# Performance work log

Measured on AMD Instinct MI355X. Metric: run time of the kernel, lower is better.

The kernel has to match this reference:

```python
import jax, jax.numpy as jnp
import numpy as np

BS = 128          # block size hard-coded in linear_deepseek_v3
FP8_MAX = 448.0   # float8_e4m3fn max-normal, used by act_quant_deepseek_v3


def act_quant(x):
    """Per-token, per-128-column-block activation quantization.
    x: [T, K] -> (xq [T, K], scale [T, K//BS]) with xq = x / scale per block."""
    T, K = x.shape
    xb = x.reshape(T, K // BS, BS)
    amax = jnp.max(jnp.abs(xb), axis=-1)              # [T, K//BS]
    scale = amax / FP8_MAX + 1e-12
    xq = (xb / scale[:, :, None]).reshape(T, K)
    return xq, scale


def linear_dsv3(x, wq, w_scale):
    """y = dequant(act_quant(x)) @ dequant(wq, w_scale).T
    x: [T, K]; wq: [N, K] fp8-style values; w_scale: [N//BS, K//BS]."""
    T, K = x.shape
    N = wq.shape[0]
    xq, xs = act_quant(x)
    # dequantized activations [T, K]
    xdq = (xq.reshape(T, K // BS, BS) * xs[:, :, None]).reshape(T, K)
    # dequantized weights [N, K] via 128x128 block scales
    wdq = (wq.reshape(N // BS, BS, K // BS, BS) * w_scale[:, None, :, None]).reshape(N, K)
    return xdq @ wdq.T


def setup_inputs() -> dict:
    key = jax.random.key(0)
    ks = jax.random.split(key, 4)
    DIM, INTER = 4096, 14336

    def make_qweight(k, n, m):
        w = jax.random.normal(k, (n, m), dtype=jnp.float32) * 0.02
        wb = w.reshape(n // BS, BS, m // BS, BS)
        amax = jnp.max(jnp.abs(wb), axis=(1, 3))       # [n//BS, m//BS]
        scale = amax / FP8_MAX + 1e-12
        wq = (wb / scale[:, None, :, None]).reshape(n, m)
        return wq, scale

    x = jax.random.normal(ks[0], (2, 1024, DIM), dtype=jnp.float32)
    w1, w1_scale = make_qweight(ks[1], INTER, DIM)
    w3, w3_scale = make_qweight(ks[2], INTER, DIM)
    w2, w2_scale = make_qweight(ks[3], DIM, INTER)
    return {"x": x, "w1": w1, "w1_scale": w1_scale, "w3": w3,
            "w3_scale": w3_scale, "w2": w2, "w2_scale": w2_scale}


def reference(x, w1, w1_scale, w3, w3_scale, w2, w2_scale):
    B, S, D = x.shape
    xf = x.reshape(-1, D)                               # [T, D]
    g = linear_dsv3(xf, w1, w1_scale)                   # gate  [T, INTER]
    u = linear_dsv3(xf, w3, w3_scale)                   # up    [T, INTER]
    h = jax.nn.silu(g) * u                              # SwiGLU
    y = linear_dsv3(h, w2, w2_scale)                    # down  [T, D]
    return y.reshape(B, S, D)
```

## Files before the change

kernel.cpp:

```cpp
#include <hip/hip_runtime.h>
#include <hip/hip_bf16.h>
#include <stdint.h>

typedef __attribute__((ext_vector_type(8))) short short8;
typedef __attribute__((ext_vector_type(4))) float f32x4;
typedef __attribute__((ext_vector_type(8))) unsigned short u16x8;

static __device__ __forceinline__ unsigned short f2bf(float f) {
  union { float f; unsigned int u; } c; c.f = f;
  unsigned int u = c.u;
  u += 0x7FFFu + ((u >> 16) & 1u);
  return (unsigned short)(u >> 16);
}
static __device__ __forceinline__ float bf2f(unsigned short h) {
  union { unsigned int u; float f; } c; c.u = ((unsigned int)h) << 16;
  return c.f;
}
static __device__ __forceinline__ f32x4 mfma_bf16(short8 a, short8 b, f32x4 c) {
  return __builtin_amdgcn_mfma_f32_16x16x32_bf16(a, b, c, 0, 0, 0);
}
static __device__ __forceinline__ void gl_lds16(const void* g, void* lds) {
  __builtin_amdgcn_global_load_lds(
      (const __attribute__((address_space(1))) void*)(unsigned long long)(uintptr_t)g,
      (__attribute__((address_space(3))) void*)(unsigned int)(uintptr_t)lds,
      16, 0, 0);
}

__global__ void k_cvt_w(const float* __restrict__ w, const float* __restrict__ s,
                        unsigned short* __restrict__ o, int N, int K) {
  const int KB = K >> 7;
  const size_t total = ((size_t)N * K) >> 3;
  for (size_t i = (size_t)blockIdx.x * blockDim.x + threadIdx.x; i < total;
       i += (size_t)gridDim.x * blockDim.x) {
    const size_t e = i << 3;
    const int n = (int)(e / K);
    const int k = (int)(e % K);
    const float sc = s[(n >> 7) * KB + (k >> 7)];
    f32x4 a = *(const f32x4*)(w + e);
    f32x4 b = *(const f32x4*)(w + e + 4);
    u16x8 q;
    #pragma unroll
    for (int j = 0; j < 4; ++j) { q[j] = f2bf(a[j] * sc); q[4 + j] = f2bf(b[j] * sc); }
    *(u16x8*)(o + e) = q;
  }
}

__global__ void k_cvt_x(const float* __restrict__ x, unsigned short* __restrict__ o,
                        size_t total8) {
  for (size_t i = (size_t)blockIdx.x * blockDim.x + threadIdx.x; i < total8;
       i += (size_t)gridDim.x * blockDim.x) {
    const size_t e = i << 3;
    f32x4 a = *(const f32x4*)(x + e);
    f32x4 b = *(const f32x4*)(x + e + 4);
    u16x8 q;
    #pragma unroll
    for (int j = 0; j < 4; ++j) { q[j] = f2bf(a[j]); q[4 + j] = f2bf(b[j]); }
    *(u16x8*)(o + e) = q;
  }
}

template<int NB, int EPI>
__global__ __launch_bounds__(512, 2)
void k_gemm256(const unsigned short* __restrict__ A,
               const unsigned short* __restrict__ B,
               const unsigned short* Gin,
               void* Out,
               int M, int N, int K) {
  constexpr int BN   = NB * 128;
  constexpr int NREP = NB * 2;
  __shared__ unsigned short lds[65536];

  const int tid  = threadIdx.x;
  const int lane = tid & 63;
  const int wid  = tid >> 6;
  const int wm   = wid >> 2;
  const int wn   = wid & 3;
  const int lr   = lane & 15;
  const int kg   = lane >> 4;
  const int xr   = (lr & 7) << 4;

  const int nwg = gridDim.x;
  const int per = nwg >> 3;
  const int wg  = (int)blockIdx.x;
  const int swz = (wg & 7) * per + (wg >> 3);
  const int bm  = swz & 7;
  const int bn  = swz >> 3;

  const int r0   = tid >> 3;
  const int colb = ((tid & 7) ^ ((tid >> 3) & 7)) << 4;
  const size_t ldb = (size_t)K * 2;

  const char* gA = (const char*)A + (size_t)bm * 256 * ldb;
  const char* gB = (const char*)B + (size_t)bn * BN * ldb;

  const int NT = K >> 6;

  auto stage = [&](int t) {
    const size_t kb = (size_t)t * 128;
    #pragma unroll
    for (int h = 0; h < 2; ++h) {
      unsigned short* d = lds + (((2 * t + h) & 3) * 8192) + wid * 512;
      const char* s = gA + (size_t)(h * 128 + r0) * ldb + kb + colb;
      gl_lds16(s,            d);
      gl_lds16(s + 64 * ldb, d + 4096);
    }
    #pragma unroll
    for (int h = 0; h < NB; ++h) {
      unsigned short* d = lds + 32768 + (((NB * t + h) & 3) * 8192) + wid * 512;
      const char* s = gB + (size_t)(h * 128 + r0) * ldb + kb + colb;
      gl_lds16(s,            d);
      gl_lds16(s + 64 * ldb, d + 4096);
    }
  };

  f32x4 acc[8][NREP];
  #pragma unroll
  for (int m = 0; m < 8; ++m)
    #pragma unroll
    for (int n = 0; n < NREP; ++n)
      #pragma unroll
      for (int e = 0; e < 4; ++e) acc[m][n][e] = 0.0f;

  const int wrow0 = (NB == 2) ? (wn & 1) * 64 : wn * 32;
  const int bhalf = (NB == 2) ? (wn >> 1) : 0;

  stage(0);
  stage(1);

  for (int t = 0; t < NT; ++t) {
    if (t == NT - 1) {
      asm volatile("s_waitcnt vmcnt(0)" ::: "memory");
    } else if constexpr (NB == 2) {
      asm volatile("s_waitcnt vmcnt(8)" ::: "memory");
    } else {
      asm volatile("s_waitcnt vmcnt(6)" ::: "memory");
    }
    __builtin_amdgcn_s_barrier();
    __builtin_amdgcn_sched_barrier(0);

    const char* ab = (const char*)lds + (((2 * t + wm) & 3) * 16384);
    const char* bb = (const char*)lds + 65536 + (((NB * t + bhalf) & 3) * 16384);

    short8 a0[8], b0[NREP], a1[8], b1[NREP];
    #pragma unroll
    for (int m = 0; m < 8; ++m)
      a0[m] = *(const short8*)(ab + ((((m * 16 + lr) * 128) + kg * 16) ^ xr));
    #pragma unroll
    for (int n = 0; n < NREP; ++n)
      b0[n] = *(const short8*)(bb + ((((wrow0 + n * 16 + lr) * 128) + kg * 16) ^ xr));
    #pragma unroll
    for (int m = 0; m < 8; ++m)
      #pragma unroll
      for (int n = 0; n < NREP; ++n)
        acc[m][n] = mfma_bf16(a0[m], b0[n], acc[m][n]);

    #pragma unroll
    for (int m = 0; m < 8; ++m)
      a1[m] = *(const short8*)(ab + ((((m * 16 + lr) * 128) + 64 + kg * 16) ^ xr));
    #pragma unroll
    for (int n = 0; n < NREP; ++n)
      b1[n] = *(const short8*)(bb + ((((wrow0 + n * 16 + lr) * 128) + 64 + kg * 16) ^ xr));

    asm volatile("s_waitcnt lgkmcnt(0)" ::: "memory");
    __builtin_amdgcn_s_barrier();
    __builtin_amdgcn_sched_barrier(0);
    if (t + 2 < NT) stage(t + 2);
    __builtin_amdgcn_sched_barrier(0);

    #pragma unroll
    for (int m = 0; m < 8; ++m)
      #pragma unroll
      for (int n = 0; n < NREP; ++n)
        acc[m][n] = mfma_bf16(a1[m], b1[n], acc[m][n]);
  }

  const int growb = bm * 256 + wm * 128 + kg * 4;
  const int gcolb = bn * BN + wn * (BN / 4) + lr;
  #pragma unroll
  for (int m = 0; m < 8; ++m)
    #pragma unroll
    for (int n = 0; n < NREP; ++n)
      #pragma unroll
      for (int j = 0; j < 4; ++j) {
        const size_t idx = (size_t)(growb + m * 16 + j) * N + (gcolb + n * 16);
        if constexpr (EPI == 0) {
          ((unsigned short*)Out)[idx] = f2bf(acc[m][n][j]);
        } else if constexpr (EPI == 1) {
          const float gv = bf2f(Gin[idx]);
          const float sg = gv / (1.0f + __expf(-gv));
          ((unsigned short*)Out)[idx] = f2bf(sg * acc[m][n][j]);
        } else {
          ((float*)Out)[idx] = acc[m][n][j];
        }
      }
}

extern "C" void kernel_launch(void* const* d_in, const int* in_sizes, int n_in,
                              void* d_out, int out_size, void* d_ws, size_t ws_size,
                              hipStream_t stream) {
  const float* x   = (const float*)d_in[0];
  const float* w1  = (const float*)d_in[1];
  const float* w1s = (const float*)d_in[2];
  const float* w3  = (const float*)d_in[3];
  const float* w3s = (const float*)d_in[4];
  const float* w2  = (const float*)d_in[5];
  const float* w2s = (const float*)d_in[6];
  float* y = (float*)d_out;

  const int D = 4096, I = 14336;
  const int T = in_sizes[0] / D;

  const size_t xbB = (size_t)T * D * 2;
  const size_t wB  = (size_t)I * D * 2;
  const size_t gB_ = (size_t)T * I * 2;

  char* ws = (char*)d_ws;
  unsigned short* xb  = (unsigned short*)(ws);
  unsigned short* w1b = (unsigned short*)(ws + xbB);
  unsigned short* w3b = (unsigned short*)(ws + xbB + wB);
  unsigned short* w2b = (unsigned short*)(ws + xbB + 2 * wB);
  unsigned short* g   = (unsigned short*)(ws + xbB + 3 * wB);

  k_cvt_x<<<2048, 256, 0, stream>>>(x, xb, ((size_t)T * D) >> 3);
  k_cvt_w<<<2048, 256, 0, stream>>>(w1, w1s, w1b, I, D);
  k_cvt_w<<<2048, 256, 0, stream>>>(w3, w3s, w3b, I, D);
  k_cvt_w<<<2048, 256, 0, stream>>>(w2, w2s, w2b, D, I);

  k_gemm256<2, 0><<<dim3((T / 256) * (I / 256)), dim3(512), 0, stream>>>(
      xb, w1b, nullptr, g, T, I, D);
  k_gemm256<2, 1><<<dim3((T / 256) * (I / 256)), dim3(512), 0, stream>>>(
      xb, w3b, g, g, T, I, D);
  k_gemm256<1, 2><<<dim3((T / 256) * (D / 128)), dim3(512), 0, stream>>>(
      g, w2b, nullptr, y, T, D, I);
}
```

Before: 907.2 us.

## Restructure GEMM main loop into 8-phase ping-pong schedule with interleaved staging

```diff
diff --git a/kernel.cpp b/kernel.cpp
--- a/kernel.cpp
+++ b/kernel.cpp
@@ -59,16 +59,57 @@
   }
 }
 
+#define PH_MID() do { \
+    __builtin_amdgcn_sched_barrier(0); \
+    __builtin_amdgcn_s_barrier(); \
+    asm volatile("s_waitcnt lgkmcnt(0)" ::: "memory"); \
+    __builtin_amdgcn_sched_barrier(0); \
+    __builtin_amdgcn_s_setprio(1); \
+  } while (0)
+#define PH_END() do { \
+    __builtin_amdgcn_s_setprio(0); \
+    __builtin_amdgcn_sched_barrier(0); \
+    __builtin_amdgcn_s_barrier(); \
+  } while (0)
+
+#define READ_A(d, mh) do { \
+    const char* _ba = (const char*)lds + ((d) * 2 + wm) * 16384; \
+    _Pragma("unroll") \
+    for (int f = 0; f < 4; ++f) { \
+      aF[0][f] = *(const short8*)(_ba + ((((mh) * 64 + f * 16 + lr) * 128 + kg * 16) ^ xr)); \
+      aF[1][f] = *(const short8*)(_ba + ((((mh) * 64 + f * 16 + lr) * 128 + 64 + kg * 16) ^ xr)); \
+    } } while (0)
+#define READ_B(d, nh, bF) do { \
+    const char* _bb = (const char*)lds + ABYTES + ((d) * NBH + bhalf) * 16384; \
+    _Pragma("unroll") \
+    for (int f = 0; f < NH2; ++f) { \
+      bF[0][f] = *(const short8*)(_bb + (((wrow0 + ((nh) * NH2 + f) * 16 + lr) * 128 + kg * 16) ^ xr)); \
+      bF[1][f] = *(const short8*)(_bb + (((wrow0 + ((nh) * NH2 + f) * 16 + lr) * 128 + 64 + kg * 16) ^ xr)); \
+    } } while (0)
+#define MFMA_Q(mh, nh, bF) do { \
+    _Pragma("unroll") \
+    for (int m = 0; m < 4; ++m) \
+      _Pragma("unroll") \
+      for (int n = 0; n < NH2; ++n) { \
+        acc[(mh) * 4 + m][(nh) * NH2 + n] = \
+            mfma_bf16(aF[0][m], bF[0][n], acc[(mh) * 4 + m][(nh) * NH2 + n]); \
+        acc[(mh) * 4 + m][(nh) * NH2 + n] = \
+            mfma_bf16(aF[1][m], bF[1][n], acc[(mh) * 4 + m][(nh) * NH2 + n]); \
+      } } while (0)
+
 template<int NB, int EPI>
 __global__ __launch_bounds__(512, 2)
-void k_gemm256(const unsigned short* __restrict__ A,
-               const unsigned short* __restrict__ B,
-               const unsigned short* Gin,
-               void* Out,
-               int M, int N, int K) {
-  constexpr int BN   = NB * 128;
-  constexpr int NREP = NB * 2;
-  __shared__ unsigned short lds[65536];
+void k_gemm8p(const unsigned short* __restrict__ A,
+              const unsigned short* __restrict__ B,
+              const unsigned short* Gin,
+              void* Out,
+              int M, int N, int K) {
+  constexpr int BN     = NB * 128;
+  constexpr int NREP   = NB * 2;
+  constexpr int NH2    = NREP / 2;
+  constexpr int NBH    = NB;
+  constexpr int ABYTES = 65536;
+  __shared__ unsigned short lds[(NB == 2) ? 65536 : 49152];
 
   const int tid  = threadIdx.x;
   const int lane = tid & 63;
@@ -93,24 +134,20 @@
   const char* gA = (const char*)A + (size_t)bm * 256 * ldb;
   const char* gB = (const char*)B + (size_t)bn * BN * ldb;
 
-  const int NT = K >> 6;
-
-  auto stage = [&](int t) {
-    const size_t kb = (size_t)t * 128;
-    #pragma unroll
-    for (int h = 0; h < 2; ++h) {
-      unsigned short* d = lds + (((2 * t + h) & 3) * 8192) + wid * 512;
-      const char* s = gA + (size_t)(h * 128 + r0) * ldb + kb + colb;
-      gl_lds16(s,            d);
-      gl_lds16(s + 64 * ldb, d + 4096);
-    }
-    #pragma unroll
-    for (int h = 0; h < NB; ++h) {
-      unsigned short* d = lds + 32768 + (((NB * t + h) & 3) * 8192) + wid * 512;
-      const char* s = gB + (size_t)(h * 128 + r0) * ldb + kb + colb;
-      gl_lds16(s,            d);
-      gl_lds16(s + 64 * ldb, d + 4096);
-    }
+  const int wrow0 = (NB == 2) ? (wn & 1) * 64 : wn * 32;
+  const int bhalf = (NB == 2) ? (wn >> 1) : 0;
+
+  auto stageA = [&](int t, int h) {
+    unsigned short* d = lds + ((t & 1) * 2 + h) * 8192 + wid * 512;
+    const char* s = gA + (size_t)(h * 128 + r0) * ldb + (size_t)t * 128 + colb;
+    gl_lds16(s, d);
+    gl_lds16(s + 64 * ldb, d + 4096);
+  };
+  auto stageB = [&](int t, int h) {
+    unsigned short* d = lds + (ABYTES / 2) + ((t & 1) * NBH + h) * 8192 + wid * 512;
+    const char* s = gB + (size_t)(h * 128 + r0) * ldb + (size_t)t * 128 + colb;
+    gl_lds16(s, d);
+    gl_lds16(s + 64 * ldb, d + 4096);
   };
 
   f32x4 acc[8][NREP];
@@ -121,57 +158,70 @@
       #pragma unroll
       for (int e = 0; e < 4; ++e) acc[m][n][e] = 0.0f;
 
-  const int wrow0 = (NB == 2) ? (wn & 1) * 64 : wn * 32;
-  const int bhalf = (NB == 2) ? (wn >> 1) : 0;
-
-  stage(0);
-  stage(1);
-
-  for (int t = 0; t < NT; ++t) {
-    if (t == NT - 1) {
+  short8 aF[2][4], bF0[2][NH2], bF1[2][NH2];
+
+  const int NP = K >> 7;
+
+  stageB(0, 0); if constexpr (NB == 2) stageB(0, 1);
+  stageA(0, 0); stageA(0, 1);
+  stageB(1, 0); if constexpr (NB == 2) stageB(1, 1);
+  stageA(1, 0); stageA(1, 1);
+  if constexpr (NB == 2) asm volatile("s_waitcnt vmcnt(8)" ::: "memory");
+  else                   asm volatile("s_waitcnt vmcnt(6)" ::: "memory");
+  __builtin_amdgcn_sched_barrier(0);
+  __builtin_amdgcn_s_barrier();
+
+  for (int i = 0; i < NP; ++i) {
+    const int t0 = 2 * i, t1 = 2 * i + 1;
+    const bool more = (i + 1 < NP);
+
+    READ_A(0, 0);
+    READ_B(0, 0, bF0);
+    if (i > 0) stageA(t1, 1);
+    PH_MID(); MFMA_Q(0, 0, bF0); PH_END();
+
+    READ_B(0, 1, bF1);
+    PH_MID(); MFMA_Q(0, 1, bF1); PH_END();
+
+    READ_A(0, 1);
+    if (more) stageB(t0 + 2, 0);
+    PH_MID(); MFMA_Q(1, 1, bF1); PH_END();
+
+    if (more) { if constexpr (NB == 2) stageB(t0 + 2, 1); stageA(t0 + 2, 0); }
+    PH_MID(); MFMA_Q(1, 0, bF0);
+    __builtin_amdgcn_s_setprio(0);
+    __builtin_amdgcn_sched_barrier(0);
+    if (more) {
+      if constexpr (NB == 2) asm volatile("s_waitcnt vmcnt(6)" ::: "memory");
+      else                   asm volatile("s_waitcnt vmcnt(4)" ::: "memory");
+    } else {
       asm volatile("s_waitcnt vmcnt(0)" ::: "memory");
-    } else if constexpr (NB == 2) {
-      asm volatile("s_waitcnt vmcnt(8)" ::: "memory");
-    } else {
-      asm volatile("s_waitcnt vmcnt(6)" ::: "memory");
     }
+    __builtin_amdgcn_sched_barrier(0);
     __builtin_amdgcn_s_barrier();
-    __builtin_amdgcn_sched_barrier(0);
-
-    const char* ab = (const char*)lds + (((2 * t + wm) & 3) * 16384);
-    const char* bb = (const char*)lds + 65536 + (((NB * t + bhalf) & 3) * 16384);
-
-    short8 a0[8], b0[NREP], a1[8], b1[NREP];
-    #pragma unroll
-    for (int m = 0; m < 8; ++m)
-      a0[m] = *(const short8*)(ab + ((((m * 16 + lr) * 128) + kg * 16) ^ xr));
-    #pragma unroll
-    for (int n = 0; n < NREP; ++n)
-      b0[n] = *(const short8*)(bb + ((((wrow0 + n * 16 + lr) * 128) + kg * 16) ^ xr));
-    #pragma unroll
-    for (int m = 0; m < 8; ++m)
-      #pragma unroll
-      for (int n = 0; n < NREP; ++n)
-        acc[m][n] = mfma_bf16(a0[m], b0[n], acc[m][n]);
-
-    #pragma unroll
-    for (int m = 0; m < 8; ++m)
-      a1[m] = *(const short8*)(ab + ((((m * 16 + lr) * 128) + 64 + kg * 16) ^ xr));
-    #pragma unroll
-    for (int n = 0; n < NREP; ++n)
-      b1[n] = *(const short8*)(bb + ((((wrow0 + n * 16 + lr) * 128) + 64 + kg * 16) ^ xr));
-
-    asm volatile("s_waitcnt lgkmcnt(0)" ::: "memory");
+
+    READ_A(1, 0);
+    READ_B(1, 0, bF0);
+    if (more) stageA(t0 + 2, 1);
+    PH_MID(); MFMA_Q(0, 0, bF0); PH_END();
+
+    READ_B(1, 1, bF1);
+    PH_MID(); MFMA_Q(0, 1, bF1); PH_END();
+
+    READ_A(1, 1);
+    if (more) stageB(t1 + 2, 0);
+    PH_MID(); MFMA_Q(1, 1, bF1); PH_END();
+
+    if (more) { if constexpr (NB == 2) stageB(t1 + 2, 1); stageA(t1 + 2, 0); }
+    PH_MID(); MFMA_Q(1, 0, bF0);
+    __builtin_amdgcn_s_setprio(0);
+    __builtin_amdgcn_sched_barrier(0);
+    if (more) {
+      if constexpr (NB == 2) asm volatile("s_waitcnt vmcnt(6)" ::: "memory");
+      else                   asm volatile("s_waitcnt vmcnt(4)" ::: "memory");
+    }
+    __builtin_amdgcn_sched_barrier(0);
     __builtin_amdgcn_s_barrier();
-    __builtin_amdgcn_sched_barrier(0);
-    if (t + 2 < NT) stage(t + 2);
-    __builtin_amdgcn_sched_barrier(0);
-
-    #pragma unroll
-    for (int m = 0; m < 8; ++m)
-      #pragma unroll
-      for (int n = 0; n < NREP; ++n)
-        acc[m][n] = mfma_bf16(a1[m], b1[n], acc[m][n]);
   }
 
   const int growb = bm * 256 + wm * 128 + kg * 4;
@@ -212,7 +262,6 @@
 
   const size_t xbB = (size_t)T * D * 2;
   const size_t wB  = (size_t)I * D * 2;
-  const size_t gB_ = (size_t)T * I * 2;
 
   char* ws = (char*)d_ws;
   unsigned short* xb  = (unsigned short*)(ws);
@@ -226,10 +275,10 @@
   k_cvt_w<<<2048, 256, 0, stream>>>(w3, w3s, w3b, I, D);
   k_cvt_w<<<2048, 256, 0, stream>>>(w2, w2s, w2b, D, I);
 
-  k_gemm256<2, 0><<<dim3((T / 256) * (I / 256)), dim3(512), 0, stream>>>(
+  k_gemm8p<2, 0><<<dim3((T / 256) * (I / 256)), dim3(512), 0, stream>>>(
       xb, w1b, nullptr, g, T, I, D);
-  k_gemm256<2, 1><<<dim3((T / 256) * (I / 256)), dim3(512), 0, stream>>>(
+  k_gemm8p<2, 1><<<dim3((T / 256) * (I / 256)), dim3(512), 0, stream>>>(
       xb, w3b, g, g, T, I, D);
-  k_gemm256<1, 2><<<dim3((T / 256) * (D / 128)), dim3(512), 0, stream>>>(
+  k_gemm8p<1, 2><<<dim3((T / 256) * (D / 128)), dim3(512), 0, stream>>>(
       g, w2b, nullptr, y, T, D, I);
 }
```

Result: slower. 938.3 us (+3.4%).

## Fuse gate and up projections into one GEMM with SwiGLU epilogue

Applied to the files above, without the earlier changes.

```diff
diff --git a/kernel.cpp b/kernel.cpp
--- a/kernel.cpp
+++ b/kernel.cpp
@@ -11,10 +11,6 @@
   unsigned int u = c.u;
   u += 0x7FFFu + ((u >> 16) & 1u);
   return (unsigned short)(u >> 16);
-}
-static __device__ __forceinline__ float bf2f(unsigned short h) {
-  union { unsigned int u; float f; } c; c.u = ((unsigned int)h) << 16;
-  return c.f;
 }
 static __device__ __forceinline__ f32x4 mfma_bf16(short8 a, short8 b, f32x4 c) {
   return __builtin_amdgcn_mfma_f32_16x16x32_bf16(a, b, c, 0, 0, 0);
@@ -59,15 +55,12 @@
   }
 }
 
-template<int NB, int EPI>
 __global__ __launch_bounds__(512, 2)
-void k_gemm256(const unsigned short* __restrict__ A,
-               const unsigned short* __restrict__ B,
-               const unsigned short* Gin,
-               void* Out,
-               int M, int N, int K) {
-  constexpr int BN   = NB * 128;
-  constexpr int NREP = NB * 2;
+void k_gateup_f(const unsigned short* __restrict__ A,
+                const unsigned short* __restrict__ B1,
+                const unsigned short* __restrict__ B3,
+                unsigned short* __restrict__ H,
+                int N, int K) {
   __shared__ unsigned short lds[65536];
 
   const int tid  = threadIdx.x;
@@ -90,10 +83,9 @@
   const int colb = ((tid & 7) ^ ((tid >> 3) & 7)) << 4;
   const size_t ldb = (size_t)K * 2;
 
-  const char* gA = (const char*)A + (size_t)bm * 256 * ldb;
-  const char* gB = (const char*)B + (size_t)bn * BN * ldb;
-
-  const int NT = K >> 6;
+  const char* gA = (const char*)A  + (size_t)bm * 256 * ldb;
+  const char* g1 = (const char*)B1 + (size_t)bn * 128 * ldb;
+  const char* g3 = (const char*)B3 + (size_t)bn * 128 * ldb;
 
   auto stage = [&](int t) {
     const size_t kb = (size_t)t * 128;
@@ -104,62 +96,69 @@
       gl_lds16(s,            d);
       gl_lds16(s + 64 * ldb, d + 4096);
     }
-    #pragma unroll
-    for (int h = 0; h < NB; ++h) {
-      unsigned short* d = lds + 32768 + (((NB * t + h) & 3) * 8192) + wid * 512;
-      const char* s = gB + (size_t)(h * 128 + r0) * ldb + kb + colb;
+    {
+      unsigned short* d = lds + 32768 + ((t & 1) * 8192) + wid * 512;
+      const char* s = g1 + (size_t)r0 * ldb + kb + colb;
+      gl_lds16(s,            d);
+      gl_lds16(s + 64 * ldb, d + 4096);
+    }
+    {
+      unsigned short* d = lds + 49152 + ((t & 1) * 8192) + wid * 512;
+      const char* s = g3 + (size_t)r0 * ldb + kb + colb;
       gl_lds16(s,            d);
       gl_lds16(s + 64 * ldb, d + 4096);
     }
   };
 
-  f32x4 acc[8][NREP];
+  f32x4 accg[8][2], accu[8][2];
   #pragma unroll
   for (int m = 0; m < 8; ++m)
     #pragma unroll
-    for (int n = 0; n < NREP; ++n)
-      #pragma unroll
-      for (int e = 0; e < 4; ++e) acc[m][n][e] = 0.0f;
-
-  const int wrow0 = (NB == 2) ? (wn & 1) * 64 : wn * 32;
-  const int bhalf = (NB == 2) ? (wn >> 1) : 0;
+    for (int n = 0; n < 2; ++n)
+      #pragma unroll
+      for (int e = 0; e < 4; ++e) { accg[m][n][e] = 0.0f; accu[m][n][e] = 0.0f; }
+
+  const int wrow0 = wn * 32;
+  const int NT = K >> 6;
 
   stage(0);
   stage(1);
 
   for (int t = 0; t < NT; ++t) {
-    if (t == NT - 1) {
-      asm volatile("s_waitcnt vmcnt(0)" ::: "memory");
-    } else if constexpr (NB == 2) {
-      asm volatile("s_waitcnt vmcnt(8)" ::: "memory");
-    } else {
-      asm volatile("s_waitcnt vmcnt(6)" ::: "memory");
-    }
+    if (t == NT - 1) asm volatile("s_waitcnt vmcnt(0)" ::: "memory");
+    else             asm volatile("s_waitcnt vmcnt(8)" ::: "memory");
     __builtin_amdgcn_s_barrier();
     __builtin_amdgcn_sched_barrier(0);
 
-    const char* ab = (const char*)lds + (((2 * t + wm) & 3) * 16384);
-    const char* bb = (const char*)lds + 65536 + (((NB * t + bhalf) & 3) * 16384);
-
-    short8 a0[8], b0[NREP], a1[8], b1[NREP];
+    const char* ab  = (const char*)lds + (((2 * t + wm) & 3) * 16384);
+    const char* b1b = (const char*)lds + 65536 + ((t & 1) * 16384);
+    const char* b3b = (const char*)lds + 98304 + ((t & 1) * 16384);
+
+    short8 a0[8], p0[2], q0[2], a1[8], p1[2], q1[2];
     #pragma unroll
     for (int m = 0; m < 8; ++m)
       a0[m] = *(const short8*)(ab + ((((m * 16 + lr) * 128) + kg * 16) ^ xr));
     #pragma unroll
-    for (int n = 0; n < NREP; ++n)
-      b0[n] = *(const short8*)(bb + ((((wrow0 + n * 16 + lr) * 128) + kg * 16) ^ xr));
-    #pragma unroll
-    for (int m = 0; m < 8; ++m)
-      #pragma unroll
-      for (int n = 0; n < NREP; ++n)
-        acc[m][n] = mfma_bf16(a0[m], b0[n], acc[m][n]);
+    for (int n = 0; n < 2; ++n) {
+      p0[n] = *(const short8*)(b1b + ((((wrow0 + n * 16 + lr) * 128) + kg * 16) ^ xr));
+      q0[n] = *(const short8*)(b3b + ((((wrow0 + n * 16 + lr) * 128) + kg * 16) ^ xr));
+    }
+    #pragma unroll
+    for (int m = 0; m < 8; ++m)
+      #pragma unroll
+      for (int n = 0; n < 2; ++n) {
+        accg[m][n] = mfma_bf16(a0[m], p0[n], accg[m][n]);
+        accu[m][n] = mfma_bf16(a0[m], q0[n], accu[m][n]);
+      }
 
     #pragma unroll
     for (int m = 0; m < 8; ++m)
       a1[m] = *(const short8*)(ab + ((((m * 16 + lr) * 128) + 64 + kg * 16) ^ xr));
     #pragma unroll
-    for (int n = 0; n < NREP; ++n)
-      b1[n] = *(const short8*)(bb + ((((wrow0 + n * 16 + lr) * 128) + 64 + kg * 16) ^ xr));
+    for (int n = 0; n < 2; ++n) {
+      p1[n] = *(const short8*)(b1b + ((((wrow0 + n * 16 + lr) * 128) + 64 + kg * 16) ^ xr));
+      q1[n] = *(const short8*)(b3b + ((((wrow0 + n * 16 + lr) * 128) + 64 + kg * 16) ^ xr));
+    }
 
     asm volatile("s_waitcnt lgkmcnt(0)" ::: "memory");
     __builtin_amdgcn_s_barrier();
@@ -170,29 +169,139 @@
     #pragma unroll
     for (int m = 0; m < 8; ++m)
       #pragma unroll
-      for (int n = 0; n < NREP; ++n)
+      for (int n = 0; n < 2; ++n) {
+        accg[m][n] = mfma_bf16(a1[m], p1[n], accg[m][n]);
+        accu[m][n] = mfma_bf16(a1[m], q1[n], accu[m][n]);
+      }
+  }
+
+  const int growb = bm * 256 + wm * 128 + kg * 4;
+  const int gcolb = bn * 128 + wn * 32 + lr;
+  #pragma unroll
+  for (int m = 0; m < 8; ++m)
+    #pragma unroll
+    for (int n = 0; n < 2; ++n)
+      #pragma unroll
+      for (int j = 0; j < 4; ++j) {
+        const float g  = accg[m][n][j];
+        const float u  = accu[m][n][j];
+        const float sg = g / (1.0f + __expf(-g));
+        H[(size_t)(growb + m * 16 + j) * N + (gcolb + n * 16)] = f2bf(sg * u);
+      }
+}
+
+__global__ __launch_bounds__(512, 2)
+void k_down256(const unsigned short* __restrict__ A,
+               const unsigned short* __restrict__ B,
+               float* __restrict__ Y,
+               int N, int K) {
+  __shared__ unsigned short lds[65536];
+
+  const int tid  = threadIdx.x;
+  const int lane = tid & 63;
+  const int wid  = tid >> 6;
+  const int wm   = wid >> 2;
+  const int wn   = wid & 3;
+  const int lr   = lane & 15;
+  const int kg   = lane >> 4;
+  const int xr   = (lr & 7) << 4;
+
+  const int nwg = gridDim.x;
+  const int per = nwg >> 3;
+  const int wg  = (int)blockIdx.x;
+  const int swz = (wg & 7) * per + (wg >> 3);
+  const int bm  = swz & 7;
+  const int bn  = swz >> 3;
+
+  const int r0   = tid >> 3;
+  const int colb = ((tid & 7) ^ ((tid >> 3) & 7)) << 4;
+  const size_t ldb = (size_t)K * 2;
+
+  const char* gA = (const char*)A + (size_t)bm * 256 * ldb;
+  const char* gB = (const char*)B + (size_t)bn * 128 * ldb;
+
+  auto stage = [&](int t) {
+    const size_t kb = (size_t)t * 128;
+    #pragma unroll
+    for (int h = 0; h < 2; ++h) {
+      unsigned short* d = lds + (((2 * t + h) & 3) * 8192) + wid * 512;
+      const char* s = gA + (size_t)(h * 128 + r0) * ldb + kb + colb;
+      gl_lds16(s,            d);
+      gl_lds16(s + 64 * ldb, d + 4096);
+    }
+    {
+      unsigned short* d = lds + 32768 + ((t & 3) * 8192) + wid * 512;
+      const char* s = gB + (size_t)r0 * ldb + kb + colb;
+      gl_lds16(s,            d);
+      gl_lds16(s + 64 * ldb, d + 4096);
+    }
+  };
+
+  f32x4 acc[8][2];
+  #pragma unroll
+  for (int m = 0; m < 8; ++m)
+    #pragma unroll
+    for (int n = 0; n < 2; ++n)
+      #pragma unroll
+      for (int e = 0; e < 4; ++e) acc[m][n][e] = 0.0f;
+
+  const int wrow0 = wn * 32;
+  const int NT = K >> 6;
+
+  stage(0);
+  stage(1);
+
+  for (int t = 0; t < NT; ++t) {
+    if (t == NT - 1) asm volatile("s_waitcnt vmcnt(0)" ::: "memory");
+    else             asm volatile("s_waitcnt vmcnt(6)" ::: "memory");
+    __builtin_amdgcn_s_barrier();
+    __builtin_amdgcn_sched_barrier(0);
+
+    const char* ab = (const char*)lds + (((2 * t + wm) & 3) * 16384);
+    const char* bb = (const char*)lds + 65536 + ((t & 3) * 16384);
+
+    short8 a0[8], b0[2], a1[8], b1[2];
+    #pragma unroll
+    for (int m = 0; m < 8; ++m)
+      a0[m] = *(const short8*)(ab + ((((m * 16 + lr) * 128) + kg * 16) ^ xr));
+    #pragma unroll
+    for (int n = 0; n < 2; ++n)
+      b0[n] = *(const short8*)(bb + ((((wrow0 + n * 16 + lr) * 128) + kg * 16) ^ xr));
+    #pragma unroll
+    for (int m = 0; m < 8; ++m)
+      #pragma unroll
+      for (int n = 0; n < 2; ++n)
+        acc[m][n] = mfma_bf16(a0[m], b0[n], acc[m][n]);
+
+    #pragma unroll
+    for (int m = 0; m < 8; ++m)
+      a1[m] = *(const short8*)(ab + ((((m * 16 + lr) * 128) + 64 + kg * 16) ^ xr));
+    #pragma unroll
+    for (int n = 0; n < 2; ++n)
+      b1[n] = *(const short8*)(bb + ((((wrow0 + n * 16 + lr) * 128) + 64 + kg * 16) ^ xr));
+
+    asm volatile("s_waitcnt lgkmcnt(0)" ::: "memory");
+    __builtin_amdgcn_s_barrier();
+    __builtin_amdgcn_sched_barrier(0);
+    if (t + 2 < NT) stage(t + 2);
+    __builtin_amdgcn_sched_barrier(0);
+
+    #pragma unroll
+    for (int m = 0; m < 8; ++m)
+      #pragma unroll
+      for (int n = 0; n < 2; ++n)
         acc[m][n] = mfma_bf16(a1[m], b1[n], acc[m][n]);
   }
 
   const int growb = bm * 256 + wm * 128 + kg * 4;
-  const int gcolb = bn * BN + wn * (BN / 4) + lr;
+  const int gcolb = bn * 128 + wn * 32 + lr;
   #pragma unroll
   for (int m = 0; m < 8; ++m)
     #pragma unroll
-    for (int n = 0; n < NREP; ++n)
-      #pragma unroll
-      for (int j = 0; j < 4; ++j) {
-        const size_t idx = (size_t)(growb + m * 16 + j) * N + (gcolb + n * 16);
-        if constexpr (EPI == 0) {
-          ((unsigned short*)Out)[idx] = f2bf(acc[m][n][j]);
-        } else if constexpr (EPI == 1) {
-          const float gv = bf2f(Gin[idx]);
-          const float sg = gv / (1.0f + __expf(-gv));
-          ((unsigned short*)Out)[idx] = f2bf(sg * acc[m][n][j]);
-        } else {
-          ((float*)Out)[idx] = acc[m][n][j];
-        }
-      }
+    for (int n = 0; n < 2; ++n)
+      #pragma unroll
+      for (int j = 0; j < 4; ++j)
+        Y[(size_t)(growb + m * 16 + j) * N + (gcolb + n * 16)] = acc[m][n][j];
 }
 
 extern "C" void kernel_launch(void* const* d_in, const int* in_sizes, int n_in,
@@ -212,24 +321,21 @@
 
   const size_t xbB = (size_t)T * D * 2;
   const size_t wB  = (size_t)I * D * 2;
-  const size_t gB_ = (size_t)T * I * 2;
 
   char* ws = (char*)d_ws;
   unsigned short* xb  = (unsigned short*)(ws);
   unsigned short* w1b = (unsigned short*)(ws + xbB);
   unsigned short* w3b = (unsigned short*)(ws + xbB + wB);
   unsigned short* w2b = (unsigned short*)(ws + xbB + 2 * wB);
-  unsigned short* g   = (unsigned short*)(ws + xbB + 3 * wB);
+  unsigned short* h   = (unsigned short*)(ws + xbB + 3 * wB);
 
   k_cvt_x<<<2048, 256, 0, stream>>>(x, xb, ((size_t)T * D) >> 3);
   k_cvt_w<<<2048, 256, 0, stream>>>(w1, w1s, w1b, I, D);
   k_cvt_w<<<2048, 256, 0, stream>>>(w3, w3s, w3b, I, D);
   k_cvt_w<<<2048, 256, 0, stream>>>(w2, w2s, w2b, D, I);
 
-  k_gemm256<2, 0><<<dim3((T / 256) * (I / 256)), dim3(512), 0, stream>>>(
-      xb, w1b, nullptr, g, T, I, D);
-  k_gemm256<2, 1><<<dim3((T / 256) * (I / 256)), dim3(512), 0, stream>>>(
-      xb, w3b, g, g, T, I, D);
-  k_gemm256<1, 2><<<dim3((T / 256) * (D / 128)), dim3(512), 0, stream>>>(
-      g, w2b, nullptr, y, T, D, I);
-}
+  k_gateup_f<<<dim3((T / 256) * (I / 128)), dim3(512), 0, stream>>>(
+      xb, w1b, w3b, h, I, D);
+  k_down256<<<dim3((T / 256) * (D / 128)), dim3(512), 0, stream>>>(
+      h, w2b, y, D, I);
+}
```

After: 856.8 us. -5.6%, faster.
